# Optimization experiments

Measured on AMD Instinct MI355X. Metric: run time of the kernel, lower is better.

Reference implementation:

```python
import jax, jax.numpy as jnp
import numpy as np

N = 100000   # nodes
E = 1600000  # edges
F_IN = 128
H = 128
C = 40


def setup_inputs() -> dict:
    key = jax.random.key(0)
    ks = jax.random.split(key, 8)
    s = 0.05
    return {
        "x": jax.random.normal(ks[0], (N, F_IN), dtype=jnp.float32),
        "edge_index": jax.random.randint(ks[1], (2, E), 0, N, dtype=jnp.int32),
        "W1": jax.random.normal(ks[2], (F_IN, H), dtype=jnp.float32) * s,
        "b1": jnp.zeros((H,), jnp.float32),
        "W2": jax.random.normal(ks[3], (H, H), dtype=jnp.float32) * s,
        "b2": jnp.zeros((H,), jnp.float32),
        "Wfc": jax.random.normal(ks[4], (H, C), dtype=jnp.float32) * s,
        "bfc": jnp.zeros((C,), jnp.float32),
    }


def _graph_conv(x, src, dst, norm_out, norm_in, W, b):
    # DGL GraphConv, norm='both': h = D_in^{-1/2} A D_out^{-1/2} x W + b
    h = (x * norm_out[:, None]) @ W                      # [N, H] (W first: in>=out)
    agg = jax.ops.segment_sum(h[src], dst, num_segments=N)  # gather + scatter-add
    return agg * norm_in[:, None] + b


def reference(x, edge_index, W1, b1, W2, b2, Wfc, bfc):
    src, dst = edge_index[0], edge_index[1]
    ones = jnp.ones((E,), x.dtype)
    deg_out = jnp.maximum(jax.ops.segment_sum(ones, src, num_segments=N), 1.0)
    deg_in = jnp.maximum(jax.ops.segment_sum(ones, dst, num_segments=N), 1.0)
    norm_out = jax.lax.rsqrt(deg_out)
    norm_in = jax.lax.rsqrt(deg_in)
    # layer 0: GraphConv + relu (dropout is identity in eval mode)
    h = jax.nn.relu(_graph_conv(x, src, dst, norm_out, norm_in, W1, b1))
    # layer 1: GraphConv, no activation
    h = _graph_conv(h, src, dst, norm_out, norm_in, W2, b2)
    # final FC
    return h @ Wfc + bfc
```

## Files before the change

kernel.cpp:

```cpp
#include <hip/hip_runtime.h>
#include <hip/hip_fp16.h>


#define CHUNK    8192
#define NB       256
#define SLAB     9216

typedef __attribute__((ext_vector_type(8))) short bf16x8;
typedef __attribute__((ext_vector_type(4))) float f32x4;

struct __align__(8)  half4 { __half x, y, z, w; };
struct __align__(16) half8 { __half h[8]; };

__device__ __forceinline__ void acc_half4(float4& acc, const half4 v) {
    acc.x += __half2float(v.x);
    acc.y += __half2float(v.y);
    acc.z += __half2float(v.z);
    acc.w += __half2float(v.w);
}

__device__ __forceinline__ unsigned short f2bf(float f) {
    union { float f; unsigned u; } v; v.f = f;
    unsigned r = v.u + 0x7FFFu + ((v.u >> 16) & 1u);
    return (unsigned short)(r >> 16);
}
__device__ __forceinline__ float bf2f(unsigned short h) {
    union { unsigned u; float f; } v; v.u = ((unsigned)h) << 16;
    return v.f;
}

__global__ void init_cursors_kernel(int* __restrict__ cur_d, int* __restrict__ cur_s,
                                    int nbuck) {
    int i = blockIdx.x * blockDim.x + threadIdx.x;
    if (i < nbuck) { cur_d[i] = i * SLAB; cur_s[i] = i * SLAB; }
}

__global__ __launch_bounds__(256) void scatter_res_kernel(
        const int* __restrict__ src, const int* __restrict__ dst,
        int* __restrict__ cur_d, int* __restrict__ cur_s,
        unsigned int* __restrict__ ppack, unsigned short* __restrict__ es_loc,
        int E) {
    __shared__ int hd[NB], hs[NB], bd[NB], bs[NB];
    const int tid = threadIdx.x;
    hd[tid] = 0; hs[tid] = 0;
    __syncthreads();
    const int base = blockIdx.x * CHUNK;
    const int end  = min(base + CHUNK, E);
    for (int e = base + tid; e < end; e += 256) {
        atomicAdd(&hd[((unsigned)dst[e]) >> 9], 1);
        atomicAdd(&hs[((unsigned)src[e]) >> 9], 1);
    }
    __syncthreads();
    int cd = hd[tid], cs = hs[tid];
    bd[tid] = cd ? atomicAdd(&cur_d[tid], cd) : 0;
    bs[tid] = cs ? atomicAdd(&cur_s[tid], cs) : 0;
    hd[tid] = 0; hs[tid] = 0;
    __syncthreads();
    for (int e = base + tid; e < end; e += 256) {
        int d = dst[e], s = src[e];
        unsigned bin_d = ((unsigned)d) >> 9;
        int pos = bd[bin_d] + atomicAdd(&hd[bin_d], 1);
        ppack[pos] = (((unsigned)d & 511u) << 17) | (unsigned)s;
        unsigned bin_s = ((unsigned)s) >> 9;
        int ps = bs[bin_s] + atomicAdd(&hs[bin_s], 1);
        es_loc[ps] = (unsigned short)(s & 511);
    }
}

__global__ __launch_bounds__(256) void fine_dst_kernel(
        const unsigned int* __restrict__ ppack, const int* __restrict__ cur_d,
        int* __restrict__ deg_in, float* __restrict__ norm_in,
        int* __restrict__ row_ptr, int* __restrict__ csr_src, int N_) {
    __shared__ int h[512];
    __shared__ int psum[256];
    const int tid = threadIdx.x;
    const int b = blockIdx.x;
    const int start = b * SLAB;
    const int end   = cur_d[b];
    const int node0 = b * 512;

    h[tid] = 0; h[tid + 256] = 0;
    __syncthreads();
    for (int i = start + tid; i < end; i += 256)
        atomicAdd(&h[ppack[i] >> 17], 1);
    __syncthreads();

    int a0 = h[2 * tid], a1 = h[2 * tid + 1];
    int pair = a0 + a1;
    psum[tid] = pair;
    __syncthreads();
    for (int off = 1; off < 256; off <<= 1) {
        int t = (tid >= off) ? psum[tid - off] : 0;
        __syncthreads();
        psum[tid] += t;
        __syncthreads();
    }
    int base0 = psum[tid] - pair + start;

    int n0 = node0 + 2 * tid, n1 = n0 + 1;
    if (n0 < N_) {
        deg_in[n0]  = a0;
        row_ptr[n0] = base0;
        norm_in[n0] = rsqrtf((float)(a0 < 1 ? 1 : a0));
    }
    if (n1 < N_) {
        deg_in[n1]  = a1;
        row_ptr[n1] = base0 + a0;
        norm_in[n1] = rsqrtf((float)(a1 < 1 ? 1 : a1));
    }
    h[2 * tid]     = base0;
    h[2 * tid + 1] = base0 + a0;
    __syncthreads();

    for (int i = start + tid; i < end; i += 256) {
        unsigned int pk = ppack[i];
        int pos = atomicAdd(&h[pk >> 17], 1);
        csr_src[pos] = (int)(pk & 0x1FFFFu);
    }
}

__global__ __launch_bounds__(256) void fine_src_kernel(
        const unsigned short* __restrict__ es_loc, const int* __restrict__ cur_s,
        float* __restrict__ norm_out, int N_) {
    __shared__ int h[512];
    const int tid = threadIdx.x;
    const int b = blockIdx.x;
    const int start = b * SLAB;
    const int end   = cur_s[b];
    const int node0 = b * 512;

    h[tid] = 0; h[tid + 256] = 0;
    __syncthreads();
    for (int i = start + tid; i < end; i += 256)
        atomicAdd(&h[es_loc[i]], 1);
    __syncthreads();

    int n0 = node0 + tid, n1 = n0 + 256;
    if (n0 < N_) { int d = h[tid];       norm_out[n0] = rsqrtf((float)(d < 1 ? 1 : d)); }
    if (n1 < N_) { int d = h[tid + 256]; norm_out[n1] = rsqrtf((float)(d < 1 ? 1 : d)); }
}

__global__ void fold_w2_kernel(const float* __restrict__ W2, const float* __restrict__ Wfc,
                               const float* __restrict__ b2, const float* __restrict__ bfc,
                               float* __restrict__ W2p, float* __restrict__ b2p) {
    int idx = blockIdx.x * blockDim.x + threadIdx.x;
    if (idx < 128 * 40) {
        int k = idx / 40, c = idx - (idx / 40) * 40;
        const float* w2row = W2 + k * 128;
        float a = 0.f;
        #pragma unroll 8
        for (int j = 0; j < 128; ++j) a += w2row[j] * Wfc[j * 40 + c];
        W2p[idx] = a;
    } else if (idx < 129 * 40) {
        int c = idx - 128 * 40;
        float a = bfc[c];
        #pragma unroll 8
        for (int j = 0; j < 128; ++j) a += b2[j] * Wfc[j * 40 + c];
        b2p[c] = a;
    }
}

__global__ __launch_bounds__(256, 2) void gemm128(
        const float* __restrict__ X, const float* __restrict__ scale,
        const float* __restrict__ W, __half* __restrict__ Y, int nrows) {
    __shared__ unsigned short wsh[128 * 128];
    __shared__ unsigned short wsl[128 * 128];
    const int tid = threadIdx.x;

    for (int i = tid; i < 4096; i += 256) {
        int k  = i >> 5;
        int n0 = (i & 31) * 4;
        float4 wv = *(const float4*)(W + k * 128 + n0);
        int q = k >> 5, j = k & 7, lb = ((k >> 3) & 3) * 16;
        int tcol = n0 >> 4;
        int base = ((tcol * 4 + q) * 64) * 8 + j;
        float vals[4] = {wv.x, wv.y, wv.z, wv.w};
        #pragma unroll
        for (int c = 0; c < 4; ++c) {
            int l = lb + ((n0 + c) & 15);
            unsigned short h = f2bf(vals[c]);
            wsh[base + l * 8] = h;
            wsl[base + l * 8] = f2bf(vals[c] - bf2f(h));
        }
    }
    __syncthreads();

    const int lane = tid & 63;
    const int w    = tid >> 6;
    const int m    = lane & 15;
    const int quad = lane >> 4;
    const int rowBase = blockIdx.x * 128 + w * 32;

    bf16x8 Ah[2][4], Al[2][4];
    #pragma unroll
    for (int rt = 0; rt < 2; ++rt) {
        int r = rowBase + rt * 16 + m;
        float sc = (r < nrows) ? scale[r] : 0.f;
        const float* xr = X + (size_t)(r < nrows ? r : 0) * 128;
        #pragma unroll
        for (int q = 0; q < 4; ++q) {
            int k0 = q * 32 + quad * 8;
            float4 a = *(const float4*)(xr + k0);
            float4 bv = *(const float4*)(xr + k0 + 4);
            float v[8] = {a.x * sc, a.y * sc, a.z * sc, a.w * sc,
                          bv.x * sc, bv.y * sc, bv.z * sc, bv.w * sc};
            bf16x8 hi, lo;
            #pragma unroll
            for (int j = 0; j < 8; ++j) {
                unsigned short h = f2bf(v[j]);
                hi[j] = (short)h;
                lo[j] = (short)f2bf(v[j] - bf2f(h));
            }
            Ah[rt][q] = hi; Al[rt][q] = lo;
        }
    }

    f32x4 acc[2][8];
    #pragma unroll
    for (int rt = 0; rt < 2; ++rt)
        #pragma unroll
        for (int t = 0; t < 8; ++t)
            acc[rt][t] = (f32x4){0.f, 0.f, 0.f, 0.f};

    #pragma unroll
    for (int t = 0; t < 8; ++t) {
        #pragma unroll
        for (int q = 0; q < 4; ++q) {
            const int off = ((t * 4 + q) * 64 + lane) * 8;
            bf16x8 Bh = *(const bf16x8*)(wsh + off);
            bf16x8 Bl = *(const bf16x8*)(wsl + off);
            #pragma unroll
            for (int rt = 0; rt < 2; ++rt) {
                acc[rt][t] = __builtin_amdgcn_mfma_f32_16x16x32_bf16(Ah[rt][q], Bh, acc[rt][t], 0, 0, 0);
                acc[rt][t] = __builtin_amdgcn_mfma_f32_16x16x32_bf16(Ah[rt][q], Bl, acc[rt][t], 0, 0, 0);
                acc[rt][t] = __builtin_amdgcn_mfma_f32_16x16x32_bf16(Al[rt][q], Bh, acc[rt][t], 0, 0, 0);
            }
        }
    }

    #pragma unroll
    for (int rt = 0; rt < 2; ++rt) {
        int r0 = rowBase + rt * 16 + quad * 4;
        #pragma unroll
        for (int reg = 0; reg < 4; ++reg) {
            int r = r0 + reg;
            if (r >= nrows) continue;
            __half* yr = Y + (size_t)r * 128 + m;
            #pragma unroll
            for (int t = 0; t < 8; ++t)
                yr[t * 16] = __float2half(acc[rt][t][reg]);
        }
    }
}

__global__ __launch_bounds__(256, 2) void gemm40(
        const __half* __restrict__ H, const float* __restrict__ scale,
        const float* __restrict__ Wp, __half* __restrict__ G, int n) {
    __shared__ unsigned short wsh[48 * 128];
    __shared__ unsigned short wsl[48 * 128];
    const int tid = threadIdx.x;

    for (int i = tid; i < 6144; i += 256) {
        int k  = i / 48;
        int nn = i - k * 48;
        float v = (nn < 40) ? Wp[k * 40 + nn] : 0.f;
        int t = nn >> 4, q = k >> 5, j = k & 7;
        int l = ((k >> 3) & 3) * 16 + (nn & 15);
        int base = ((t * 4 + q) * 64 + l) * 8 + j;
        unsigned short h = f2bf(v);
        wsh[base] = h;
        wsl[base] = f2bf(v - bf2f(h));
    }
    __syncthreads();

    const int lane = tid & 63;
    const int w    = tid >> 6;
    const int m    = lane & 15;
    const int quad = lane >> 4;
    const int rowBase = blockIdx.x * 128 + w * 32;

    bf16x8 Ah[2][4], Al[2][4];
    #pragma unroll
    for (int rt = 0; rt < 2; ++rt) {
        int r = rowBase + rt * 16 + m;
        float sc = (r < n) ? scale[r] : 0.f;
        const __half* xr = H + (size_t)(r < n ? r : 0) * 128;
        #pragma unroll
        for (int q = 0; q < 4; ++q) {
            int k0 = q * 32 + quad * 8;
            half4 a = *(const half4*)(xr + k0);
            half4 bv = *(const half4*)(xr + k0 + 4);
            float v[8] = {__half2float(a.x) * sc, __half2float(a.y) * sc,
                          __half2float(a.z) * sc, __half2float(a.w) * sc,
                          __half2float(bv.x) * sc, __half2float(bv.y) * sc,
                          __half2float(bv.z) * sc, __half2float(bv.w) * sc};
            bf16x8 hi, lo;
            #pragma unroll
            for (int j = 0; j < 8; ++j) {
                unsigned short h = f2bf(v[j]);
                hi[j] = (short)h;
                lo[j] = (short)f2bf(v[j] - bf2f(h));
            }
            Ah[rt][q] = hi; Al[rt][q] = lo;
        }
    }

    f32x4 acc[2][3];
    #pragma unroll
    for (int rt = 0; rt < 2; ++rt)
        #pragma unroll
        for (int t = 0; t < 3; ++t)
            acc[rt][t] = (f32x4){0.f, 0.f, 0.f, 0.f};

    #pragma unroll
    for (int t = 0; t < 3; ++t) {
        #pragma unroll
        for (int q = 0; q < 4; ++q) {
            const int off = ((t * 4 + q) * 64 + lane) * 8;
            bf16x8 Bh = *(const bf16x8*)(wsh + off);
            bf16x8 Bl = *(const bf16x8*)(wsl + off);
            #pragma unroll
            for (int rt = 0; rt < 2; ++rt) {
                acc[rt][t] = __builtin_amdgcn_mfma_f32_16x16x32_bf16(Ah[rt][q], Bh, acc[rt][t], 0, 0, 0);
                acc[rt][t] = __builtin_amdgcn_mfma_f32_16x16x32_bf16(Ah[rt][q], Bl, acc[rt][t], 0, 0, 0);
                acc[rt][t] = __builtin_amdgcn_mfma_f32_16x16x32_bf16(Al[rt][q], Bh, acc[rt][t], 0, 0, 0);
            }
        }
    }

    #pragma unroll
    for (int rt = 0; rt < 2; ++rt) {
        int r0 = rowBase + rt * 16 + quad * 4;
        #pragma unroll
        for (int reg = 0; reg < 4; ++reg) {
            int r = r0 + reg;
            if (r >= n) continue;
            __half* gr = G + (size_t)r * 40;
            #pragma unroll
            for (int t = 0; t < 3; ++t) {
                int col = t * 16 + m;
                if (col < 40) gr[col] = __float2half(acc[rt][t][reg]);
            }
        }
    }
}

__global__ __launch_bounds__(256) void gather_kernel(
        const __half* __restrict__ H, const int* __restrict__ row_ptr,
        const int* __restrict__ deg, const int* __restrict__ csr_src,
        const float* __restrict__ norm_in, const float* __restrict__ b,
        __half* __restrict__ out, int n) {
    const int tid  = threadIdx.x;
    const int node = blockIdx.x * 8 + (tid >> 5);
    const int c    = (tid & 31) * 4;
    if (node >= n) return;

    const int start = row_ptr[node];
    const int cnt   = deg[node];
    float4 acc = make_float4(0.f, 0.f, 0.f, 0.f);

    int j = 0;
    for (; j + 8 <= cnt; j += 8) {
        int s0 = csr_src[start + j];
        int s1 = csr_src[start + j + 1];
        int s2 = csr_src[start + j + 2];
        int s3 = csr_src[start + j + 3];
        int s4 = csr_src[start + j + 4];
        int s5 = csr_src[start + j + 5];
        int s6 = csr_src[start + j + 6];
        int s7 = csr_src[start + j + 7];
        half4 v0 = *(const half4*)(H + (long long)s0 * 128 + c);
        half4 v1 = *(const half4*)(H + (long long)s1 * 128 + c);
        half4 v2 = *(const half4*)(H + (long long)s2 * 128 + c);
        half4 v3 = *(const half4*)(H + (long long)s3 * 128 + c);
        half4 v4 = *(const half4*)(H + (long long)s4 * 128 + c);
        half4 v5 = *(const half4*)(H + (long long)s5 * 128 + c);
        half4 v6 = *(const half4*)(H + (long long)s6 * 128 + c);
        half4 v7 = *(const half4*)(H + (long long)s7 * 128 + c);
        acc_half4(acc, v0); acc_half4(acc, v1); acc_half4(acc, v2); acc_half4(acc, v3);
        acc_half4(acc, v4); acc_half4(acc, v5); acc_half4(acc, v6); acc_half4(acc, v7);
    }
    for (; j + 4 <= cnt; j += 4) {
        int s0 = csr_src[start + j];
        int s1 = csr_src[start + j + 1];
        int s2 = csr_src[start + j + 2];
        int s3 = csr_src[start + j + 3];
        half4 v0 = *(const half4*)(H + (long long)s0 * 128 + c);
        half4 v1 = *(const half4*)(H + (long long)s1 * 128 + c);
        half4 v2 = *(const half4*)(H + (long long)s2 * 128 + c);
        half4 v3 = *(const half4*)(H + (long long)s3 * 128 + c);
        acc_half4(acc, v0); acc_half4(acc, v1); acc_half4(acc, v2); acc_half4(acc, v3);
    }
    for (; j < cnt; ++j) {
        int s0 = csr_src[start + j];
        half4 v0 = *(const half4*)(H + (long long)s0 * 128 + c);
        acc_half4(acc, v0);
    }

    float ni = norm_in[node];
    float4 bb = *(const float4*)(b + c);
    half4 o;
    o.x = __float2half(fmaxf(acc.x * ni + bb.x, 0.f));
    o.y = __float2half(fmaxf(acc.y * ni + bb.y, 0.f));
    o.z = __float2half(fmaxf(acc.z * ni + bb.z, 0.f));
    o.w = __float2half(fmaxf(acc.w * ni + bb.w, 0.f));
    *(half4*)(out + (long long)node * 128 + c) = o;
}

__global__ __launch_bounds__(256) void gather40_kernel(
        const __half* __restrict__ G, const int* __restrict__ row_ptr,
        const int* __restrict__ deg, const int* __restrict__ csr_src,
        const float* __restrict__ norm_in, const float* __restrict__ b2p,
        float* __restrict__ out, int n) {
    const int t = blockIdx.x * 256 + threadIdx.x;
    if (t >= n * 5) return;
    const int node = t / 5;
    const int c    = (t - node * 5) * 8;

    const int start = row_ptr[node];
    const int cnt   = deg[node];
    float acc[8] = {0.f, 0.f, 0.f, 0.f, 0.f, 0.f, 0.f, 0.f};

    int j = 0;
    for (; j + 4 <= cnt; j += 4) {
        int s0 = csr_src[start + j];
        int s1 = csr_src[start + j + 1];
        int s2 = csr_src[start + j + 2];
        int s3 = csr_src[start + j + 3];
        half8 v0 = *(const half8*)(G + (long long)s0 * 40 + c);
        half8 v1 = *(const half8*)(G + (long long)s1 * 40 + c);
        half8 v2 = *(const half8*)(G + (long long)s2 * 40 + c);
        half8 v3 = *(const half8*)(G + (long long)s3 * 40 + c);
        #pragma unroll
        for (int k = 0; k < 8; ++k)
            acc[k] += (__half2float(v0.h[k]) + __half2float(v1.h[k]))
                    + (__half2float(v2.h[k]) + __half2float(v3.h[k]));
    }
    for (; j < cnt; ++j) {
        int s0 = csr_src[start + j];
        half8 v0 = *(const half8*)(G + (long long)s0 * 40 + c);
        #pragma unroll
        for (int k = 0; k < 8; ++k) acc[k] += __half2float(v0.h[k]);
    }

    float ni = norm_in[node];
    float4 o0, o1;
    o0.x = acc[0] * ni + b2p[c + 0];
    o0.y = acc[1] * ni + b2p[c + 1];
    o0.z = acc[2] * ni + b2p[c + 2];
    o0.w = acc[3] * ni + b2p[c + 3];
    o1.x = acc[4] * ni + b2p[c + 4];
    o1.y = acc[5] * ni + b2p[c + 5];
    o1.z = acc[6] * ni + b2p[c + 6];
    o1.w = acc[7] * ni + b2p[c + 7];
    float* op = out + (long long)node * 40 + c;
    *(float4*)(op)     = o0;
    *(float4*)(op + 4) = o1;
}

extern "C" void kernel_launch(void* const* d_in, const int* in_sizes, int n_in,
                              void* d_out, int out_size, void* d_ws, size_t ws_size,
                              hipStream_t stream) {
    const float* x   = (const float*)d_in[0];
    const int*   ei  = (const int*)  d_in[1];
    const float* W1  = (const float*)d_in[2];
    const float* b1  = (const float*)d_in[3];
    const float* W2  = (const float*)d_in[4];
    const float* b2  = (const float*)d_in[5];
    const float* Wfc = (const float*)d_in[6];
    const float* bfc = (const float*)d_in[7];
    float* out = (float*)d_out;

    const int N = in_sizes[0] / 128;
    const int E = in_sizes[1] / 2;
    const int* src = ei;
    const int* dst = ei + E;

    const int nbuck = (N + 511) >> 9;
    const int B1 = (E + CHUNK - 1) / CHUNK;

    char* p = (char*)d_ws;
    float* norm_out = (float*)p; p += (size_t)N * 4;
    float* norm_in  = (float*)p; p += (size_t)N * 4;
    float* bufA     = (float*)p; p += (size_t)N * 128 * 4;
    float* bufB     = (float*)p; p += (size_t)N * 128 * 4;
    int*   deg_in   = (int*)p;   p += (size_t)N * 4;
    int*   row_ptr  = (int*)p;   p += (size_t)N * 4;
    int*   csr_src  = (int*)p;   p += (size_t)nbuck * SLAB * 4;
    int*   cur_d    = (int*)p;   p += (size_t)1024 * 4;
    int*   cur_s    = (int*)p;   p += (size_t)1024 * 4;
    float* W2p      = (float*)p; p += (size_t)128 * 40 * 4;
    float* b2p      = (float*)p; p += (size_t)64 * 4;

    unsigned int*   ppack  = (unsigned int*)bufB;
    unsigned short* es_loc = (unsigned short*)(ppack + (size_t)nbuck * SLAB);

    __half* h1pre = (__half*)bufA;
    __half* G     = (__half*)bufA;
    __half* h1    = (__half*)bufB;

    const int T = 256;

    init_cursors_kernel<<<(nbuck + T - 1) / T, T, 0, stream>>>(cur_d, cur_s, nbuck);
    scatter_res_kernel<<<B1, T, 0, stream>>>(src, dst, cur_d, cur_s, ppack, es_loc, E);
    fine_dst_kernel<<<nbuck, T, 0, stream>>>(ppack, cur_d, deg_in, norm_in,
                                             row_ptr, csr_src, N);
    fine_src_kernel<<<nbuck, T, 0, stream>>>(es_loc, cur_s, norm_out, N);

    fold_w2_kernel<<<(129 * 40 + T - 1) / T, T, 0, stream>>>(W2, Wfc, b2, bfc, W2p, b2p);

    const int gemm_grid = (N + 127) / 128;
    gemm128<<<gemm_grid, T, 0, stream>>>(x, norm_out, W1, h1pre, N);
    const int gather_grid = (N + 7) / 8;
    gather_kernel<<<gather_grid, T, 0, stream>>>(h1pre, row_ptr, deg_in, csr_src,
                                                 norm_in, b1, h1, N);
    gemm40<<<gemm_grid, T, 0, stream>>>(h1, norm_out, W2p, G, N);
    gather40_kernel<<<((size_t)N * 5 + T - 1) / T, T, 0, stream>>>(
        G, row_ptr, deg_in, csr_src, norm_in, b2p, out, N);
}
```

Baseline: 323.2 us.

## Fuse layer-1 gather into layer-2 GEMM and merge preprocessing kernels

Fuses the layer-1 neighbor gather (with relu and bias) into the gemm40 kernel. Each block aggregates its 128 nodes into an LDS tile and feeds that tile straight to the MFMA GEMM, so the h1 intermediate no longer makes a global write and read. It also merges the cursor init with the W2/Wfc fold into one kernel, and merges the dst and src fine-bucketing kernels into one, cutting launches. CHUNK is halved to give the scatter more blocks. The cost is that the gather now runs inside a GEMM kernel that uses more LDS and has launch bounds (256,2), so less gather parallelism may hide latency.

```diff
diff --git a/kernel.cpp b/kernel.cpp
--- a/kernel.cpp
+++ b/kernel.cpp
@@ -2,7 +2,7 @@
 #include <hip/hip_fp16.h>
 
 
-#define CHUNK    8192
+#define CHUNK    4096
 #define NB       256
 #define SLAB     9216
 
@@ -29,123 +29,14 @@
     return v.f;
 }
 
-__global__ void init_cursors_kernel(int* __restrict__ cur_d, int* __restrict__ cur_s,
-                                    int nbuck) {
-    int i = blockIdx.x * blockDim.x + threadIdx.x;
-    if (i < nbuck) { cur_d[i] = i * SLAB; cur_s[i] = i * SLAB; }
-}
-
-__global__ __launch_bounds__(256) void scatter_res_kernel(
-        const int* __restrict__ src, const int* __restrict__ dst,
-        int* __restrict__ cur_d, int* __restrict__ cur_s,
-        unsigned int* __restrict__ ppack, unsigned short* __restrict__ es_loc,
-        int E) {
-    __shared__ int hd[NB], hs[NB], bd[NB], bs[NB];
-    const int tid = threadIdx.x;
-    hd[tid] = 0; hs[tid] = 0;
-    __syncthreads();
-    const int base = blockIdx.x * CHUNK;
-    const int end  = min(base + CHUNK, E);
-    for (int e = base + tid; e < end; e += 256) {
-        atomicAdd(&hd[((unsigned)dst[e]) >> 9], 1);
-        atomicAdd(&hs[((unsigned)src[e]) >> 9], 1);
-    }
-    __syncthreads();
-    int cd = hd[tid], cs = hs[tid];
-    bd[tid] = cd ? atomicAdd(&cur_d[tid], cd) : 0;
-    bs[tid] = cs ? atomicAdd(&cur_s[tid], cs) : 0;
-    hd[tid] = 0; hs[tid] = 0;
-    __syncthreads();
-    for (int e = base + tid; e < end; e += 256) {
-        int d = dst[e], s = src[e];
-        unsigned bin_d = ((unsigned)d) >> 9;
-        int pos = bd[bin_d] + atomicAdd(&hd[bin_d], 1);
-        ppack[pos] = (((unsigned)d & 511u) << 17) | (unsigned)s;
-        unsigned bin_s = ((unsigned)s) >> 9;
-        int ps = bs[bin_s] + atomicAdd(&hs[bin_s], 1);
-        es_loc[ps] = (unsigned short)(s & 511);
-    }
-}
-
-__global__ __launch_bounds__(256) void fine_dst_kernel(
-        const unsigned int* __restrict__ ppack, const int* __restrict__ cur_d,
-        int* __restrict__ deg_in, float* __restrict__ norm_in,
-        int* __restrict__ row_ptr, int* __restrict__ csr_src, int N_) {
-    __shared__ int h[512];
-    __shared__ int psum[256];
-    const int tid = threadIdx.x;
-    const int b = blockIdx.x;
-    const int start = b * SLAB;
-    const int end   = cur_d[b];
-    const int node0 = b * 512;
-
-    h[tid] = 0; h[tid + 256] = 0;
-    __syncthreads();
-    for (int i = start + tid; i < end; i += 256)
-        atomicAdd(&h[ppack[i] >> 17], 1);
-    __syncthreads();
-
-    int a0 = h[2 * tid], a1 = h[2 * tid + 1];
-    int pair = a0 + a1;
-    psum[tid] = pair;
-    __syncthreads();
-    for (int off = 1; off < 256; off <<= 1) {
-        int t = (tid >= off) ? psum[tid - off] : 0;
-        __syncthreads();
-        psum[tid] += t;
-        __syncthreads();
-    }
-    int base0 = psum[tid] - pair + start;
-
-    int n0 = node0 + 2 * tid, n1 = n0 + 1;
-    if (n0 < N_) {
-        deg_in[n0]  = a0;
-        row_ptr[n0] = base0;
-        norm_in[n0] = rsqrtf((float)(a0 < 1 ? 1 : a0));
-    }
-    if (n1 < N_) {
-        deg_in[n1]  = a1;
-        row_ptr[n1] = base0 + a0;
-        norm_in[n1] = rsqrtf((float)(a1 < 1 ? 1 : a1));
-    }
-    h[2 * tid]     = base0;
-    h[2 * tid + 1] = base0 + a0;
-    __syncthreads();
-
-    for (int i = start + tid; i < end; i += 256) {
-        unsigned int pk = ppack[i];
-        int pos = atomicAdd(&h[pk >> 17], 1);
-        csr_src[pos] = (int)(pk & 0x1FFFFu);
-    }
-}
-
-__global__ __launch_bounds__(256) void fine_src_kernel(
-        const unsigned short* __restrict__ es_loc, const int* __restrict__ cur_s,
-        float* __restrict__ norm_out, int N_) {
-    __shared__ int h[512];
-    const int tid = threadIdx.x;
-    const int b = blockIdx.x;
-    const int start = b * SLAB;
-    const int end   = cur_s[b];
-    const int node0 = b * 512;
-
-    h[tid] = 0; h[tid + 256] = 0;
-    __syncthreads();
-    for (int i = start + tid; i < end; i += 256)
-        atomicAdd(&h[es_loc[i]], 1);
-    __syncthreads();
-
-    int n0 = node0 + tid, n1 = n0 + 256;
-    if (n0 < N_) { int d = h[tid];       norm_out[n0] = rsqrtf((float)(d < 1 ? 1 : d)); }
-    if (n1 < N_) { int d = h[tid + 256]; norm_out[n1] = rsqrtf((float)(d < 1 ? 1 : d)); }
-}
-
-__global__ void fold_w2_kernel(const float* __restrict__ W2, const float* __restrict__ Wfc,
-                               const float* __restrict__ b2, const float* __restrict__ bfc,
-                               float* __restrict__ W2p, float* __restrict__ b2p) {
+__global__ void setup_kernel(const float* __restrict__ W2, const float* __restrict__ Wfc,
+                             const float* __restrict__ b2, const float* __restrict__ bfc,
+                             float* __restrict__ W2p, float* __restrict__ b2p,
+                             int* __restrict__ cur_d, int* __restrict__ cur_s, int nbuck) {
     int idx = blockIdx.x * blockDim.x + threadIdx.x;
+    if (idx < nbuck) { cur_d[idx] = idx * SLAB; cur_s[idx] = idx * SLAB; }
     if (idx < 128 * 40) {
-        int k = idx / 40, c = idx - (idx / 40) * 40;
+        int k = idx / 40, c = idx - k * 40;
         const float* w2row = W2 + k * 128;
         float a = 0.f;
         #pragma unroll 8
@@ -158,6 +49,104 @@
         for (int j = 0; j < 128; ++j) a += b2[j] * Wfc[j * 40 + c];
         b2p[c] = a;
     }
+}
+
+__global__ __launch_bounds__(256) void scatter_res_kernel(
+        const int* __restrict__ src, const int* __restrict__ dst,
+        int* __restrict__ cur_d, int* __restrict__ cur_s,
+        unsigned int* __restrict__ ppack, unsigned short* __restrict__ es_loc,
+        int E) {
+    __shared__ int hd[NB], hs[NB], bd[NB], bs[NB];
+    const int tid = threadIdx.x;
+    hd[tid] = 0; hs[tid] = 0;
+    __syncthreads();
+    const int base = blockIdx.x * CHUNK;
+    const int end  = min(base + CHUNK, E);
+    for (int e = base + tid; e < end; e += 256) {
+        atomicAdd(&hd[((unsigned)dst[e]) >> 9], 1);
+        atomicAdd(&hs[((unsigned)src[e]) >> 9], 1);
+    }
+    __syncthreads();
+    int cd = hd[tid], cs = hs[tid];
+    bd[tid] = cd ? atomicAdd(&cur_d[tid], cd) : 0;
+    bs[tid] = cs ? atomicAdd(&cur_s[tid], cs) : 0;
+    hd[tid] = 0; hs[tid] = 0;
+    __syncthreads();
+    for (int e = base + tid; e < end; e += 256) {
+        int d = dst[e], s = src[e];
+        unsigned bin_d = ((unsigned)d) >> 9;
+        int pos = bd[bin_d] + atomicAdd(&hd[bin_d], 1);
+        ppack[pos] = (((unsigned)d & 511u) << 17) | (unsigned)s;
+        unsigned bin_s = ((unsigned)s) >> 9;
+        int ps = bs[bin_s] + atomicAdd(&hs[bin_s], 1);
+        es_loc[ps] = (unsigned short)(s & 511);
+    }
+}
+
+__global__ __launch_bounds__(256) void fine_kernel(
+        const unsigned int* __restrict__ ppack, const unsigned short* __restrict__ es_loc,
+        const int* __restrict__ cur_d, const int* __restrict__ cur_s,
+        int* __restrict__ deg_in, float* __restrict__ norm_in,
+        int* __restrict__ row_ptr, int* __restrict__ csr_src,
+        float* __restrict__ norm_out, int N_) {
+    __shared__ int h[512];
+    __shared__ int psum[256];
+    const int tid = threadIdx.x;
+    const int b = blockIdx.x;
+    const int start = b * SLAB;
+    const int node0 = b * 512;
+
+    const int end_d = cur_d[b];
+    h[tid] = 0; h[tid + 256] = 0;
+    __syncthreads();
+    for (int i = start + tid; i < end_d; i += 256)
+        atomicAdd(&h[ppack[i] >> 17], 1);
+    __syncthreads();
+
+    int a0 = h[2 * tid], a1 = h[2 * tid + 1];
+    int pair = a0 + a1;
+    psum[tid] = pair;
+    __syncthreads();
+    for (int off = 1; off < 256; off <<= 1) {
+        int t = (tid >= off) ? psum[tid - off] : 0;
+        __syncthreads();
+        psum[tid] += t;
+        __syncthreads();
+    }
+    int base0 = psum[tid] - pair + start;
+
+    int n0 = node0 + 2 * tid, n1 = n0 + 1;
+    if (n0 < N_) {
+        deg_in[n0]  = a0;
+        row_ptr[n0] = base0;
+        norm_in[n0] = rsqrtf((float)(a0 < 1 ? 1 : a0));
+    }
+    if (n1 < N_) {
+        deg_in[n1]  = a1;
+        row_ptr[n1] = base0 + a0;
+        norm_in[n1] = rsqrtf((float)(a1 < 1 ? 1 : a1));
+    }
+    h[2 * tid]     = base0;
+    h[2 * tid + 1] = base0 + a0;
+    __syncthreads();
+
+    for (int i = start + tid; i < end_d; i += 256) {
+        unsigned int pk = ppack[i];
+        int pos = atomicAdd(&h[pk >> 17], 1);
+        csr_src[pos] = (int)(pk & 0x1FFFFu);
+    }
+    __syncthreads();
+
+    const int end_s = cur_s[b];
+    h[tid] = 0; h[tid + 256] = 0;
+    __syncthreads();
+    for (int i = start + tid; i < end_s; i += 256)
+        atomicAdd(&h[es_loc[i]], 1);
+    __syncthreads();
+
+    n0 = node0 + tid; n1 = n0 + 256;
+    if (n0 < N_) { int d = h[tid];       norm_out[n0] = rsqrtf((float)(d < 1 ? 1 : d)); }
+    if (n1 < N_) { int d = h[tid + 256]; norm_out[n1] = rsqrtf((float)(d < 1 ? 1 : d)); }
 }
 
 __global__ __launch_bounds__(256, 2) void gemm128(
@@ -253,12 +242,17 @@
     }
 }
 
-__global__ __launch_bounds__(256, 2) void gemm40(
-        const __half* __restrict__ H, const float* __restrict__ scale,
-        const float* __restrict__ Wp, __half* __restrict__ G, int n) {
+__global__ __launch_bounds__(256, 2) void layer2_fused(
+        const __half* __restrict__ H, const int* __restrict__ row_ptr,
+        const int* __restrict__ deg, const int* __restrict__ csr_src,
+        const float* __restrict__ norm_in, const float* __restrict__ b1,
+        const float* __restrict__ norm_out, const float* __restrict__ Wp,
+        __half* __restrict__ G, int n) {
     __shared__ unsigned short wsh[48 * 128];
     __shared__ unsigned short wsl[48 * 128];
+    __shared__ __half tile[4][128][32];
     const int tid = threadIdx.x;
+    const int node0 = blockIdx.x * 128;
 
     for (int i = tid; i < 6144; i += 256) {
         int k  = i / 48;
@@ -271,35 +265,90 @@
         wsh[base] = h;
         wsl[base] = f2bf(v - bf2f(h));
     }
+
+    const int c  = (tid & 31) * 4;
+    const int qc = c >> 5;
+    const int cc = c & 31;
+    for (int it = 0; it < 16; ++it) {
+        int nl   = it * 8 + (tid >> 5);
+        int node = node0 + nl;
+        half4 o;
+        if (node < n) {
+            const int start = row_ptr[node];
+            const int cnt   = deg[node];
+            float4 acc = make_float4(0.f, 0.f, 0.f, 0.f);
+            int j = 0;
+            for (; j + 8 <= cnt; j += 8) {
+                int s0 = csr_src[start + j];
+                int s1 = csr_src[start + j + 1];
+                int s2 = csr_src[start + j + 2];
+                int s3 = csr_src[start + j + 3];
+                int s4 = csr_src[start + j + 4];
+                int s5 = csr_src[start + j + 5];
+                int s6 = csr_src[start + j + 6];
+                int s7 = csr_src[start + j + 7];
+                half4 v0 = *(const half4*)(H + (long long)s0 * 128 + c);
+                half4 v1 = *(const half4*)(H + (long long)s1 * 128 + c);
+                half4 v2 = *(const half4*)(H + (long long)s2 * 128 + c);
+                half4 v3 = *(const half4*)(H + (long long)s3 * 128 + c);
+                half4 v4 = *(const half4*)(H + (long long)s4 * 128 + c);
+                half4 v5 = *(const half4*)(H + (long long)s5 * 128 + c);
+                half4 v6 = *(const half4*)(H + (long long)s6 * 128 + c);
+                half4 v7 = *(const half4*)(H + (long long)s7 * 128 + c);
+                acc_half4(acc, v0); acc_half4(acc, v1); acc_half4(acc, v2); acc_half4(acc, v3);
+                acc_half4(acc, v4); acc_half4(acc, v5); acc_half4(acc, v6); acc_half4(acc, v7);
+            }
+            for (; j + 4 <= cnt; j += 4) {
+                int s0 = csr_src[start + j];
+                int s1 = csr_src[start + j + 1];
+                int s2 = csr_src[start + j + 2];
+                int s3 = csr_src[start + j + 3];
+                half4 v0 = *(const half4*)(H + (long long)s0 * 128 + c);
+                half4 v1 = *(const half4*)(H + (long long)s1 * 128 + c);
+                half4 v2 = *(const half4*)(H + (long long)s2 * 128 + c);
+                half4 v3 = *(const half4*)(H + (long long)s3 * 128 + c);
+                acc_half4(acc, v0); acc_half4(acc, v1); acc_half4(acc, v2); acc_half4(acc, v3);
+            }
+            for (; j < cnt; ++j) {
+                int s0 = csr_src[start + j];
+                half4 v0 = *(const half4*)(H + (long long)s0 * 128 + c);
+                acc_half4(acc, v0);
+            }
+            float ni = norm_in[node];
+            float4 bb = *(const float4*)(b1 + c);
+            o.x = __float2half(fmaxf(acc.x * ni + bb.x, 0.f));
+            o.y = __float2half(fmaxf(acc.y * ni + bb.y, 0.f));
+            o.z = __float2half(fmaxf(acc.z * ni + bb.z, 0.f));
+            o.w = __float2half(fmaxf(acc.w * ni + bb.w, 0.f));
+        } else {
+            o.x = __float2half(0.f); o.y = o.x; o.z = o.x; o.w = o.x;
+        }
+        *(half4*)(&tile[qc][nl][cc]) = o;
+    }
     __syncthreads();
 
     const int lane = tid & 63;
     const int w    = tid >> 6;
     const int m    = lane & 15;
     const int quad = lane >> 4;
-    const int rowBase = blockIdx.x * 128 + w * 32;
+    const int rb   = w * 32;
 
     bf16x8 Ah[2][4], Al[2][4];
     #pragma unroll
     for (int rt = 0; rt < 2; ++rt) {
-        int r = rowBase + rt * 16 + m;
-        float sc = (r < n) ? scale[r] : 0.f;
-        const __half* xr = H + (size_t)(r < n ? r : 0) * 128;
+        int rl = rb + rt * 16 + m;
+        int r  = node0 + rl;
+        float sc = (r < n) ? norm_out[r] : 0.f;
         #pragma unroll
         for (int q = 0; q < 4; ++q) {
-            int k0 = q * 32 + quad * 8;
-            half4 a = *(const half4*)(xr + k0);
-            half4 bv = *(const half4*)(xr + k0 + 4);
-            float v[8] = {__half2float(a.x) * sc, __half2float(a.y) * sc,
-                          __half2float(a.z) * sc, __half2float(a.w) * sc,
-                          __half2float(bv.x) * sc, __half2float(bv.y) * sc,
-                          __half2float(bv.z) * sc, __half2float(bv.w) * sc};
+            half8 hv = *(const half8*)(&tile[q][rl][quad * 8]);
             bf16x8 hi, lo;
             #pragma unroll
             for (int j = 0; j < 8; ++j) {
-                unsigned short h = f2bf(v[j]);
+                float v = __half2float(hv.h[j]) * sc;
+                unsigned short h = f2bf(v);
                 hi[j] = (short)h;
-                lo[j] = (short)f2bf(v[j] - bf2f(h));
+                lo[j] = (short)f2bf(v - bf2f(h));
             }
             Ah[rt][q] = hi; Al[rt][q] = lo;
         }
@@ -330,7 +379,7 @@
 
     #pragma unroll
     for (int rt = 0; rt < 2; ++rt) {
-        int r0 = rowBase + rt * 16 + quad * 4;
+        int r0 = node0 + rb + rt * 16 + quad * 4;
         #pragma unroll
         for (int reg = 0; reg < 4; ++reg) {
             int r = r0 + reg;
@@ -343,68 +392,6 @@
             }
         }
     }
-}
-
-__global__ __launch_bounds__(256) void gather_kernel(
-        const __half* __restrict__ H, const int* __restrict__ row_ptr,
-        const int* __restrict__ deg, const int* __restrict__ csr_src,
-        const float* __restrict__ norm_in, const float* __restrict__ b,
-        __half* __restrict__ out, int n) {
-    const int tid  = threadIdx.x;
-    const int node = blockIdx.x * 8 + (tid >> 5);
-    const int c    = (tid & 31) * 4;
-    if (node >= n) return;
-
-    const int start = row_ptr[node];
-    const int cnt   = deg[node];
-    float4 acc = make_float4(0.f, 0.f, 0.f, 0.f);
-
-    int j = 0;
-    for (; j + 8 <= cnt; j += 8) {
-        int s0 = csr_src[start + j];
-        int s1 = csr_src[start + j + 1];
-        int s2 = csr_src[start + j + 2];
-        int s3 = csr_src[start + j + 3];
-        int s4 = csr_src[start + j + 4];
-        int s5 = csr_src[start + j + 5];
-        int s6 = csr_src[start + j + 6];
-        int s7 = csr_src[start + j + 7];
-        half4 v0 = *(const half4*)(H + (long long)s0 * 128 + c);
-        half4 v1 = *(const half4*)(H + (long long)s1 * 128 + c);
-        half4 v2 = *(const half4*)(H + (long long)s2 * 128 + c);
-        half4 v3 = *(const half4*)(H + (long long)s3 * 128 + c);
-        half4 v4 = *(const half4*)(H + (long long)s4 * 128 + c);
-        half4 v5 = *(const half4*)(H + (long long)s5 * 128 + c);
-        half4 v6 = *(const half4*)(H + (long long)s6 * 128 + c);
-        half4 v7 = *(const half4*)(H + (long long)s7 * 128 + c);
-        acc_half4(acc, v0); acc_half4(acc, v1); acc_half4(acc, v2); acc_half4(acc, v3);
-        acc_half4(acc, v4); acc_half4(acc, v5); acc_half4(acc, v6); acc_half4(acc, v7);
-    }
-    for (; j + 4 <= cnt; j += 4) {
-        int s0 = csr_src[start + j];
-        int s1 = csr_src[start + j + 1];
-        int s2 = csr_src[start + j + 2];
-        int s3 = csr_src[start + j + 3];
-        half4 v0 = *(const half4*)(H + (long long)s0 * 128 + c);
-        half4 v1 = *(const half4*)(H + (long long)s1 * 128 + c);
-        half4 v2 = *(const half4*)(H + (long long)s2 * 128 + c);
-        half4 v3 = *(const half4*)(H + (long long)s3 * 128 + c);
-        acc_half4(acc, v0); acc_half4(acc, v1); acc_half4(acc, v2); acc_half4(acc, v3);
-    }
-    for (; j < cnt; ++j) {
-        int s0 = csr_src[start + j];
-        half4 v0 = *(const half4*)(H + (long long)s0 * 128 + c);
-        acc_half4(acc, v0);
-    }
-
-    float ni = norm_in[node];
-    float4 bb = *(const float4*)(b + c);
-    half4 o;
-    o.x = __float2half(fmaxf(acc.x * ni + bb.x, 0.f));
-    o.y = __float2half(fmaxf(acc.y * ni + bb.y, 0.f));
-    o.z = __float2half(fmaxf(acc.z * ni + bb.z, 0.f));
-    o.w = __float2half(fmaxf(acc.w * ni + bb.w, 0.f));
-    *(half4*)(out + (long long)node * 128 + c) = o;
 }
 
 __global__ __launch_bounds__(256) void gather40_kernel(
@@ -496,25 +483,23 @@
     unsigned short* es_loc = (unsigned short*)(ppack + (size_t)nbuck * SLAB);
 
     __half* h1pre = (__half*)bufA;
-    __half* G     = (__half*)bufA;
-    __half* h1    = (__half*)bufB;
+    __half* G     = (__half*)bufB;
 
     const int T = 256;
 
-    init_cursors_kernel<<<(nbuck + T - 1) / T, T, 0, stream>>>(cur_d, cur_s, nbuck);
+    setup_kernel<<<(129 * 40 + T - 1) / T, T, 0, stream>>>(
+        W2, Wfc, b2, bfc, W2p, b2p, cur_d, cur_s, nbuck);
     scatter_res_kernel<<<B1, T, 0, stream>>>(src, dst, cur_d, cur_s, ppack, es_loc, E);
-    fine_dst_kernel<<<nbuck, T, 0, stream>>>(ppack, cur_d, deg_in, norm_in,
-                                             row_ptr, csr_src, N);
-    fine_src_kernel<<<nbuck, T, 0, stream>>>(es_loc, cur_s, norm_out, N);
-
-    fold_w2_kernel<<<(129 * 40 + T - 1) / T, T, 0, stream>>>(W2, Wfc, b2, bfc, W2p, b2p);
+    fine_kernel<<<nbuck, T, 0, stream>>>(ppack, es_loc, cur_d, cur_s,
+                                         deg_in, norm_in, row_ptr, csr_src,
+                                         norm_out, N);
 
     const int gemm_grid = (N + 127) / 128;
     gemm128<<<gemm_grid, T, 0, stream>>>(x, norm_out, W1, h1pre, N);
-    const int gather_grid = (N + 7) / 8;
-    gather_kernel<<<gather_grid, T, 0, stream>>>(h1pre, row_ptr, deg_in, csr_src,
-                                                 norm_in, b1, h1, N);
-    gemm40<<<gemm_grid, T, 0, stream>>>(h1, norm_out, W2p, G, N);
+
+    layer2_fused<<<gemm_grid, T, 0, stream>>>(h1pre, row_ptr, deg_in, csr_src,
+                                              norm_in, b1, norm_out, W2p, G, N);
+
     gather40_kernel<<<((size_t)N * 5 + T - 1) / T, T, 0, stream>>>(
         G, row_ptr, deg_in, csr_src, norm_in, b2p, out, N);
 }
```

After: 393.9 us. 21.9% more time.

## Widen gather loads to half8, fuse setup kernels, halve scatter chunk

Applied to the files above, without the earlier changes.

The layer-1 gather now gives each thread 8 half channels loaded as 16-byte vectors, so 16 lanes cover a node and a block handles 16 nodes. The 8-way unrolled edge loop is dropped and four neighbours are summed pairwise per step. Cursor init and the W2·Wfc fold are merged into one kernel to save a launch. The scatter chunk size is halved so more blocks share the binning work. Wider loads cut the number of gather instructions, but each node now has fewer edge loads in flight, and the smaller chunk adds more global cursor atomics.

```diff
diff --git a/kernel.cpp b/kernel.cpp
--- a/kernel.cpp
+++ b/kernel.cpp
@@ -2,7 +2,7 @@
 #include <hip/hip_fp16.h>
 
 
-#define CHUNK    8192
+#define CHUNK    4096
 #define NB       256
 #define SLAB     9216
 
@@ -11,13 +11,6 @@
 
 struct __align__(8)  half4 { __half x, y, z, w; };
 struct __align__(16) half8 { __half h[8]; };
-
-__device__ __forceinline__ void acc_half4(float4& acc, const half4 v) {
-    acc.x += __half2float(v.x);
-    acc.y += __half2float(v.y);
-    acc.z += __half2float(v.z);
-    acc.w += __half2float(v.w);
-}
 
 __device__ __forceinline__ unsigned short f2bf(float f) {
     union { float f; unsigned u; } v; v.f = f;
@@ -29,10 +22,26 @@
     return v.f;
 }
 
-__global__ void init_cursors_kernel(int* __restrict__ cur_d, int* __restrict__ cur_s,
-                                    int nbuck) {
-    int i = blockIdx.x * blockDim.x + threadIdx.x;
-    if (i < nbuck) { cur_d[i] = i * SLAB; cur_s[i] = i * SLAB; }
+__global__ void setup_kernel(const float* __restrict__ W2, const float* __restrict__ Wfc,
+                             const float* __restrict__ b2, const float* __restrict__ bfc,
+                             float* __restrict__ W2p, float* __restrict__ b2p,
+                             int* __restrict__ cur_d, int* __restrict__ cur_s, int nbuck) {
+    int idx = blockIdx.x * blockDim.x + threadIdx.x;
+    if (idx < nbuck) { cur_d[idx] = idx * SLAB; cur_s[idx] = idx * SLAB; }
+    if (idx < 128 * 40) {
+        int k = idx / 40, c = idx - k * 40;
+        const float* w2row = W2 + k * 128;
+        float a = 0.f;
+        #pragma unroll 8
+        for (int j = 0; j < 128; ++j) a += w2row[j] * Wfc[j * 40 + c];
+        W2p[idx] = a;
+    } else if (idx < 129 * 40) {
+        int c = idx - 128 * 40;
+        float a = bfc[c];
+        #pragma unroll 8
+        for (int j = 0; j < 128; ++j) a += b2[j] * Wfc[j * 40 + c];
+        b2p[c] = a;
+    }
 }
 
 __global__ __launch_bounds__(256) void scatter_res_kernel(
@@ -140,26 +149,6 @@
     if (n1 < N_) { int d = h[tid + 256]; norm_out[n1] = rsqrtf((float)(d < 1 ? 1 : d)); }
 }
 
-__global__ void fold_w2_kernel(const float* __restrict__ W2, const float* __restrict__ Wfc,
-                               const float* __restrict__ b2, const float* __restrict__ bfc,
-                               float* __restrict__ W2p, float* __restrict__ b2p) {
-    int idx = blockIdx.x * blockDim.x + threadIdx.x;
-    if (idx < 128 * 40) {
-        int k = idx / 40, c = idx - (idx / 40) * 40;
-        const float* w2row = W2 + k * 128;
-        float a = 0.f;
-        #pragma unroll 8
-        for (int j = 0; j < 128; ++j) a += w2row[j] * Wfc[j * 40 + c];
-        W2p[idx] = a;
-    } else if (idx < 129 * 40) {
-        int c = idx - 128 * 40;
-        float a = bfc[c];
-        #pragma unroll 8
-        for (int j = 0; j < 128; ++j) a += b2[j] * Wfc[j * 40 + c];
-        b2p[c] = a;
-    }
-}
-
 __global__ __launch_bounds__(256, 2) void gemm128(
         const float* __restrict__ X, const float* __restrict__ scale,
         const float* __restrict__ W, __half* __restrict__ Y, int nrows) {
@@ -351,60 +340,49 @@
         const float* __restrict__ norm_in, const float* __restrict__ b,
         __half* __restrict__ out, int n) {
     const int tid  = threadIdx.x;
-    const int node = blockIdx.x * 8 + (tid >> 5);
-    const int c    = (tid & 31) * 4;
+    const int node = blockIdx.x * 16 + (tid >> 4);
+    const int c    = (tid & 15) * 8;
     if (node >= n) return;
 
     const int start = row_ptr[node];
     const int cnt   = deg[node];
-    float4 acc = make_float4(0.f, 0.f, 0.f, 0.f);
+    float acc[8] = {0.f, 0.f, 0.f, 0.f, 0.f, 0.f, 0.f, 0.f};
 
     int j = 0;
-    for (; j + 8 <= cnt; j += 8) {
-        int s0 = csr_src[start + j];
-        int s1 = csr_src[start + j + 1];
-        int s2 = csr_src[start + j + 2];
-        int s3 = csr_src[start + j + 3];
-        int s4 = csr_src[start + j + 4];
-        int s5 = csr_src[start + j + 5];
-        int s6 = csr_src[start + j + 6];
-        int s7 = csr_src[start + j + 7];
-        half4 v0 = *(const half4*)(H + (long long)s0 * 128 + c);
-        half4 v1 = *(const half4*)(H + (long long)s1 * 128 + c);
-        half4 v2 = *(const half4*)(H + (long long)s2 * 128 + c);
-        half4 v3 = *(const half4*)(H + (long long)s3 * 128 + c);
-        half4 v4 = *(const half4*)(H + (long long)s4 * 128 + c);
-        half4 v5 = *(const half4*)(H + (long long)s5 * 128 + c);
-        half4 v6 = *(const half4*)(H + (long long)s6 * 128 + c);
-        half4 v7 = *(const half4*)(H + (long long)s7 * 128 + c);
-        acc_half4(acc, v0); acc_half4(acc, v1); acc_half4(acc, v2); acc_half4(acc, v3);
-        acc_half4(acc, v4); acc_half4(acc, v5); acc_half4(acc, v6); acc_half4(acc, v7);
-    }
     for (; j + 4 <= cnt; j += 4) {
         int s0 = csr_src[start + j];
         int s1 = csr_src[start + j + 1];
         int s2 = csr_src[start + j + 2];
         int s3 = csr_src[start + j + 3];
-        half4 v0 = *(const half4*)(H + (long long)s0 * 128 + c);
-        half4 v1 = *(const half4*)(H + (long long)s1 * 128 + c);
-        half4 v2 = *(const half4*)(H + (long long)s2 * 128 + c);
-        half4 v3 = *(const half4*)(H + (long long)s3 * 128 + c);
-        acc_half4(acc, v0); acc_half4(acc, v1); acc_half4(acc, v2); acc_half4(acc, v3);
+        half8 v0 = *(const half8*)(H + (long long)s0 * 128 + c);
+        half8 v1 = *(const half8*)(H + (long long)s1 * 128 + c);
+        half8 v2 = *(const half8*)(H + (long long)s2 * 128 + c);
+        half8 v3 = *(const half8*)(H + (long long)s3 * 128 + c);
+        #pragma unroll
+        for (int k = 0; k < 8; ++k)
+            acc[k] += (__half2float(v0.h[k]) + __half2float(v1.h[k]))
+                    + (__half2float(v2.h[k]) + __half2float(v3.h[k]));
     }
     for (; j < cnt; ++j) {
         int s0 = csr_src[start + j];
-        half4 v0 = *(const half4*)(H + (long long)s0 * 128 + c);
-        acc_half4(acc, v0);
+        half8 v0 = *(const half8*)(H + (long long)s0 * 128 + c);
+        #pragma unroll
+        for (int k = 0; k < 8; ++k) acc[k] += __half2float(v0.h[k]);
     }
 
     float ni = norm_in[node];
-    float4 bb = *(const float4*)(b + c);
-    half4 o;
-    o.x = __float2half(fmaxf(acc.x * ni + bb.x, 0.f));
-    o.y = __float2half(fmaxf(acc.y * ni + bb.y, 0.f));
-    o.z = __float2half(fmaxf(acc.z * ni + bb.z, 0.f));
-    o.w = __float2half(fmaxf(acc.w * ni + bb.w, 0.f));
-    *(half4*)(out + (long long)node * 128 + c) = o;
+    float4 b0 = *(const float4*)(b + c);
+    float4 b1v = *(const float4*)(b + c + 4);
+    half8 o;
+    o.h[0] = __float2half(fmaxf(acc[0] * ni + b0.x, 0.f));
+    o.h[1] = __float2half(fmaxf(acc[1] * ni + b0.y, 0.f));
+    o.h[2] = __float2half(fmaxf(acc[2] * ni + b0.z, 0.f));
+    o.h[3] = __float2half(fmaxf(acc[3] * ni + b0.w, 0.f));
+    o.h[4] = __float2half(fmaxf(acc[4] * ni + b1v.x, 0.f));
+    o.h[5] = __float2half(fmaxf(acc[5] * ni + b1v.y, 0.f));
+    o.h[6] = __float2half(fmaxf(acc[6] * ni + b1v.z, 0.f));
+    o.h[7] = __float2half(fmaxf(acc[7] * ni + b1v.w, 0.f));
+    *(half8*)(out + (long long)node * 128 + c) = o;
 }
 
 __global__ __launch_bounds__(256) void gather40_kernel(
@@ -501,17 +479,16 @@
 
     const int T = 256;
 
-    init_cursors_kernel<<<(nbuck + T - 1) / T, T, 0, stream>>>(cur_d, cur_s, nbuck);
+    setup_kernel<<<(129 * 40 + T - 1) / T, T, 0, stream>>>(
+        W2, Wfc, b2, bfc, W2p, b2p, cur_d, cur_s, nbuck);
     scatter_res_kernel<<<B1, T, 0, stream>>>(src, dst, cur_d, cur_s, ppack, es_loc, E);
     fine_dst_kernel<<<nbuck, T, 0, stream>>>(ppack, cur_d, deg_in, norm_in,
                                              row_ptr, csr_src, N);
     fine_src_kernel<<<nbuck, T, 0, stream>>>(es_loc, cur_s, norm_out, N);
 
-    fold_w2_kernel<<<(129 * 40 + T - 1) / T, T, 0, stream>>>(W2, Wfc, b2, bfc, W2p, b2p);
-
     const int gemm_grid = (N + 127) / 128;
     gemm128<<<gemm_grid, T, 0, stream>>>(x, norm_out, W1, h1pre, N);
-    const int gather_grid = (N + 7) / 8;
+    const int gather_grid = (N + 15) / 16;
     gather_kernel<<<gather_grid, T, 0, stream>>>(h1pre, row_ptr, deg_in, csr_src,
                                                  norm_in, b1, h1, N);
     gemm40<<<gemm_grid, T, 0, stream>>>(h1, norm_out, W2p, G, N);
```

Measured after the change: 322.0 us. No clear change (-0.4%).
